# Kernel tuning notes

Hardware: AMD Instinct MI355X
Metric: run time of the kernel (lower is better)

Reference implementation:

```python
import jax, jax.numpy as jnp
import numpy as np

B, T, C = 4, 128, 512
NH, HS = 8, 64          # n_head, head_dim = C // NH
ORDER = 3               # attention_order
SCALE = 1.0 / np.sqrt(HS)


def setup_inputs() -> dict:
    key = jax.random.key(0)
    ks = jax.random.split(key, 7)
    s = 0.02
    return {
        "x": jax.random.normal(ks[0], (B, T, C), jnp.float32),
        "Wp0": jax.random.normal(ks[1], (C, C), jnp.float32) * s,
        "Wp1": jax.random.normal(ks[2], (C, C), jnp.float32) * s,
        "Wp2": jax.random.normal(ks[3], (C, C), jnp.float32) * s,
        "Wv0": jax.random.normal(ks[4], (HS, HS), jnp.float32) * s,
        "Wv1": jax.random.normal(ks[5], (HS, HS), jnp.float32) * s,
        "Wc": jax.random.normal(ks[6], (C, C), jnp.float32) * s,
    }


def _heads(x, W):
    # Linear then split heads: (B,T,C) -> (B,NH,T,HS)
    return (x @ W).reshape(B, T, NH, HS).transpose(0, 2, 1, 3)


def _causal_mask(t, order):
    # indices grid [T]^order, True where i0 >= i1 >= ... >= i_{order-1}
    idx = jnp.arange(t)
    g = jnp.stack(jnp.meshgrid(*([idx] * order), indexing='ij'), axis=-1)
    return jnp.all(jnp.diff(g, axis=-1) <= 0, axis=-1)


def reference(x, Wp0, Wp1, Wp2, Wv0, Wv1, Wc):
    p0 = _heads(x, Wp0)  # (B,NH,T,HS)
    p1 = _heads(x, Wp1)
    p2 = _heads(x, Wp2)

    # pairwise scores, then higher-order broadcast exactly as the torch einsum
    # ('bh...i,bhkd->bh...ik' sums the key over d and broadcasts — faithful).
    att = jnp.einsum('bhid,bhjd->bhij', p0, p1) * SCALE        # (B,NH,T,T)
    att = jnp.einsum('bh...i,bhkd->bh...ik', att, p2)          # (B,NH,T,T,T)

    mask = _causal_mask(T, ORDER)[None, None]                  # (1,1,T,T,T)
    att = jnp.where(mask, att, -jnp.inf)
    att = jax.nn.softmax(att.reshape(B, NH, T, T * T), axis=-1)

    # value tensors with broadcasted elementwise product over the order dims
    V0 = (p1 @ Wv0)[:, :, :, None, :]   # (B,NH,T,1,HS)
    V1 = (p2 @ Wv1)[:, :, None, :, :]   # (B,NH,1,T,HS)
    V = (V0 * V1).reshape(B, NH, T * T, HS)

    y = jnp.einsum('bhij,bhjd->bhid', att, V)                  # (B,NH,T,HS)
    y = y.transpose(0, 2, 1, 3).reshape(B, T, C)
    return y @ Wc
```

## Files before the change

### kernel.cpp

```cpp
#include <hip/hip_runtime.h>
#include <hip/hip_bf16.h>
#include <math.h>

#define B 4
#define T 128
#define C 512
#define NH 8
#define HS 64
#define BH (B*NH)

typedef __attribute__((ext_vector_type(8))) short bf16x8;
typedef __attribute__((ext_vector_type(4))) float f32x4;

__device__ __forceinline__ unsigned short bfc(float x) {
    return __builtin_bit_cast(unsigned short, __float2bfloat16(x));
}
__device__ __forceinline__ unsigned int pk_bf16(float a, float b) {
    return (unsigned int)bfc(a) | ((unsigned int)bfc(b) << 16);
}
__device__ __forceinline__ float lo_f(unsigned int g) {
    return __builtin_bit_cast(float, g << 16);
}
__device__ __forceinline__ float hi_f(unsigned int g) {
    return __builtin_bit_cast(float, g & 0xffff0000u);
}

__global__ __launch_bounds__(256) void proj_kernel(
    const float* __restrict__ X,
    const float* __restrict__ Wp0, const float* __restrict__ Wp1, const float* __restrict__ Wp2,
    unsigned short* __restrict__ p0b, unsigned short* __restrict__ p1b,
    unsigned short* __restrict__ p2b, float* __restrict__ rr)
{
    __shared__ __align__(16) unsigned short As[32][72];
    __shared__ __align__(16) unsigned short Bs[64][72];
    __shared__ float Ls[64][69];
    __shared__ float sRS[4][32];
    const int z = blockIdx.z;
    const float* W = (z == 0) ? Wp0 : (z == 1) ? Wp1 : Wp2;
    const int m0 = blockIdx.y * 32, n0 = blockIdx.x * 64;
    const int tid = threadIdx.x;
    const int w = tid >> 6, lane = tid & 63, quad = lane >> 4, l16 = lane & 15;
    f32x4 acc[2];
    #pragma unroll
    for (int mt = 0; mt < 2; ++mt) acc[mt] = (f32x4){0.f, 0.f, 0.f, 0.f};

    for (int k0 = 0; k0 < 512; k0 += 64) {
        __syncthreads();
        {
            const int row = tid >> 3, c8 = (tid & 7) * 8;
            const float4 a = *(const float4*)&X[(size_t)(m0 + row) * 512 + k0 + c8];
            const float4 b = *(const float4*)&X[(size_t)(m0 + row) * 512 + k0 + c8 + 4];
            uint4 o;
            o.x = pk_bf16(a.x, a.y);
            o.y = pk_bf16(a.z, a.w);
            o.z = pk_bf16(b.x, b.y);
            o.w = pk_bf16(b.z, b.w);
            *(uint4*)&As[row][c8] = o;
        }
        #pragma unroll
        for (int it = 0; it < 4; ++it) {
            const int q = tid + it * 256;
            const int row = q >> 4, c4 = (q & 15) * 4;
            const float4 v = *(const float4*)&W[(size_t)(k0 + row) * 512 + n0 + c4];
            Ls[row][c4 + 0] = v.x; Ls[row][c4 + 1] = v.y;
            Ls[row][c4 + 2] = v.z; Ls[row][c4 + 3] = v.w;
        }
        __syncthreads();
        #pragma unroll
        for (int it = 0; it < 2; ++it) {
            const int q = tid + it * 256;
            const int nrow = q >> 3, k8 = (q & 7) * 8;
            uint4 o;
            o.x = pk_bf16(Ls[k8 + 0][nrow], Ls[k8 + 1][nrow]);
            o.y = pk_bf16(Ls[k8 + 2][nrow], Ls[k8 + 3][nrow]);
            o.z = pk_bf16(Ls[k8 + 4][nrow], Ls[k8 + 5][nrow]);
            o.w = pk_bf16(Ls[k8 + 6][nrow], Ls[k8 + 7][nrow]);
            *(uint4*)&Bs[nrow][k8] = o;
        }
        __syncthreads();
        #pragma unroll
        for (int kt = 0; kt < 2; ++kt) {
            const bf16x8 b8 = *(const bf16x8*)&Bs[w * 16 + l16][kt * 32 + quad * 8];
            #pragma unroll
            for (int mt = 0; mt < 2; ++mt) {
                const bf16x8 a8 = *(const bf16x8*)&As[mt * 16 + l16][kt * 32 + quad * 8];
                acc[mt] = __builtin_amdgcn_mfma_f32_16x16x32_bf16(a8, b8, acc[mt], 0, 0, 0);
            }
        }
    }

    {
        const int n = n0 + w * 16 + l16;
        const int h = n >> 6, d = n & 63;
        unsigned short* pz = (z == 0) ? p0b : (z == 1) ? p1b : p2b;
        #pragma unroll
        for (int mt = 0; mt < 2; ++mt) {
            #pragma unroll
            for (int r = 0; r < 4; ++r) {
                const int m = m0 + mt * 16 + quad * 4 + r;
                const int bb = m >> 7, t = m & 127;
                pz[((size_t)(bb * NH + h) * T + t) * HS + d] = bfc(acc[mt][r]);
            }
        }
    }
    if (z == 2) {
        #pragma unroll
        for (int mt = 0; mt < 2; ++mt)
            #pragma unroll
            for (int r = 0; r < 4; ++r) {
                float v = acc[mt][r];
                v += __shfl_xor(v, 1, 64); v += __shfl_xor(v, 2, 64);
                v += __shfl_xor(v, 4, 64); v += __shfl_xor(v, 8, 64);
                if (l16 == 0) sRS[w][mt * 16 + quad * 4 + r] = v;
            }
        __syncthreads();
        if (tid < 32) {
            const float s = sRS[0][tid] + sRS[1][tid] + sRS[2][tid] + sRS[3][tid];
            const int m = m0 + tid, bb = m >> 7, tl = m & 127, h = n0 >> 6;
            rr[(bb * NH + h) * T + tl] = s;
        }
    }
}

__global__ __launch_bounds__(512, 4) void attn_kernel(
    const unsigned short* __restrict__ p0b, const unsigned short* __restrict__ p1b,
    const unsigned short* __restrict__ p2b, const float* __restrict__ rr,
    const float* __restrict__ Wv0, const float* __restrict__ Wv1,
    unsigned short* __restrict__ Yb)
{
    __shared__ __align__(16) union {
        struct {
            unsigned short sWv[64][72];
            unsigned short sVst[64][136];
        } v;
        unsigned short sE[2][128 * 128];
    } u;
    __shared__ float sS[8][128];
    __shared__ float srr[128];
    __shared__ float sZarr[8][8];
    __shared__ float sY[8][2][64];

    const int bid = blockIdx.x;
    const int bh = bid & (BH - 1);
    const int ig = bid >> 5;
    const int tid = threadIdx.x;
    const int w = tid >> 6;
    const int lane = tid & 63;
    const int quad = lane >> 4;
    const int l16 = lane & 15;
    const int wq = w & 3;
    const int h4 = (w >> 2) * 4;

    if (tid < 128) srr[tid] = rr[bh * T + tid];

    #pragma unroll
    for (int it = 0; it < 2; ++it) {
        const int k = (tid >> 4) + it * 32;
        const int d0 = (tid & 15) * 4;
        const float4 wv = *(const float4*)&Wv0[(size_t)k * 64 + d0];
        u.v.sWv[d0 + 0][k] = bfc(wv.x); u.v.sWv[d0 + 1][k] = bfc(wv.y);
        u.v.sWv[d0 + 2][k] = bfc(wv.z); u.v.sWv[d0 + 3][k] = bfc(wv.w);
    }
    __syncthreads();

    {
        f32x4 vacc[4];
        #pragma unroll
        for (int mt = 0; mt < 4; ++mt) vacc[mt] = (f32x4){0.f, 0.f, 0.f, 0.f};
        #pragma unroll
        for (int kt = 0; kt < 2; ++kt) {
            const bf16x8 b8 = *(const bf16x8*)&p1b[((size_t)bh * T + w * 16 + l16) * HS + kt * 32 + quad * 8];
            #pragma unroll
            for (int mt = 0; mt < 4; ++mt) {
                const bf16x8 a8 = *(const bf16x8*)&u.v.sWv[mt * 16 + l16][kt * 32 + quad * 8];
                vacc[mt] = __builtin_amdgcn_mfma_f32_16x16x32_bf16(a8, b8, vacc[mt], 0, 0, 0);
            }
        }
        #pragma unroll
        for (int mt = 0; mt < 4; ++mt)
            #pragma unroll
            for (int r = 0; r < 4; ++r)
                u.v.sVst[mt * 16 + quad * 4 + r][w * 16 + l16] = bfc(vacc[mt][r]);
    }
    __syncthreads();

    uint2 v0r[4];
    #pragma unroll
    for (int m = 0; m < 4; ++m)
        v0r[m] = *(const uint2*)&u.v.sVst[(wq << 4) + l16][((h4 + m) << 4) + (quad << 2)];
    #pragma unroll
    for (int it = 0; it < 2; ++it) {
        const int k = (tid >> 4) + it * 32;
        const int d0 = (tid & 15) * 4;
        const float4 wv = *(const float4*)&Wv1[(size_t)k * 64 + d0];
        u.v.sWv[d0 + 0][k] = bfc(wv.x); u.v.sWv[d0 + 1][k] = bfc(wv.y);
        u.v.sWv[d0 + 2][k] = bfc(wv.z); u.v.sWv[d0 + 3][k] = bfc(wv.w);
    }
    __syncthreads();

    {
        f32x4 vacc[4];
        #pragma unroll
        for (int mt = 0; mt < 4; ++mt) vacc[mt] = (f32x4){0.f, 0.f, 0.f, 0.f};
        #pragma unroll
        for (int kt = 0; kt < 2; ++kt) {
            const bf16x8 b8 = *(const bf16x8*)&p2b[((size_t)bh * T + w * 16 + l16) * HS + kt * 32 + quad * 8];
            #pragma unroll
            for (int mt = 0; mt < 4; ++mt) {
                const bf16x8 a8 = *(const bf16x8*)&u.v.sWv[mt * 16 + l16][kt * 32 + quad * 8];
                vacc[mt] = __builtin_amdgcn_mfma_f32_16x16x32_bf16(a8, b8, vacc[mt], 0, 0, 0);
            }
        }
        #pragma unroll
        for (int mt = 0; mt < 4; ++mt)
            #pragma unroll
            for (int r = 0; r < 4; ++r)
                u.v.sVst[mt * 16 + quad * 4 + r][w * 16 + l16] = bfc(vacc[mt][r]);
    }
    __syncthreads();

    uint4 v1r[4];
    #pragma unroll
    for (int kt = 0; kt < 4; ++kt)
        v1r[kt] = *(const uint4*)&u.v.sVst[(wq << 4) + l16][(quad << 3) + (kt << 5)];
    {
        const int qr = l16 & 7;
        const int irow = (qr & 1) ? (16 * qr + 15 - ig) : (16 * qr + ig);
        const unsigned short* ap = p0b + ((size_t)bh * T + irow) * HS + (quad << 3);
        const unsigned short* bp = p1b + (size_t)bh * T * HS + (quad << 3);
        f32x4 s0 = (f32x4){0.f, 0.f, 0.f, 0.f};
        #pragma unroll
        for (int kt = 0; kt < 2; ++kt) {
            const bf16x8 a8 = *(const bf16x8*)(ap + (kt << 5));
            const bf16x8 b0 = *(const bf16x8*)(bp + (size_t)((w << 4) + l16) * HS + (kt << 5));
            s0 = __builtin_amdgcn_mfma_f32_16x16x32_bf16(a8, b0, s0, 0, 0, 0);
        }
        if (quad < 2) {
            #pragma unroll
            for (int r = 0; r < 4; ++r)
                sS[quad * 4 + r][(w << 4) + l16] = s0[r] * 0.125f;
        }
    }
    __syncthreads();

    const float L2E = 1.4426950408889634f;

    float mhat;
    {
        float aS = 0.f;
        #pragma unroll
        for (int q = 0; q < 8; ++q) {
            aS = fmaxf(aS, fabsf(sS[q][lane]));
            aS = fmaxf(aS, fabsf(sS[q][64 + lane]));
        }
        float aR = fmaxf(fabsf(srr[lane]), fabsf(srr[64 + lane]));
        #pragma unroll
        for (int off = 32; off; off >>= 1) {
            aS = fmaxf(aS, __shfl_xor(aS, off, 64));
            aR = fmaxf(aR, __shfl_xor(aR, off, 64));
        }
        mhat = aS * aR;
    }
    const float bexp = -mhat * L2E;
    const int cc = tid & 15;
    const int rowin = tid >> 4;
    const int k0l = cc << 3;
    float rk[8];
    *(float4*)&rk[0] = *(const float4*)&srr[k0l];
    *(float4*)&rk[4] = *(const float4*)&srr[k0l + 4];

    for (int qq = 7; qq >= 0; --qq) {
        const int i = (qq & 1) ? (16 * qq + 15 - ig) : (16 * qq + ig);
        const float* sSq = sS[qq];
        const int mtmax = i >> 4;
        const int buf = qq & 1;
        float zacc = 0.f;

        const int npass = (mtmax + 2) >> 1;
        for (int p = 0; p < npass; ++p) {
            const int jj = (p << 5) + rowin;
            uint4 o = {0u, 0u, 0u, 0u};
            if (jj <= i && k0l <= jj) {
                const float aL = sSq[jj] * L2E;
                const int dlim = jj - k0l;
                float e[8];
                #pragma unroll
                for (int q = 0; q < 8; ++q) {
                    const float ex = __builtin_amdgcn_exp2f(fmaf(aL, rk[q], bexp));
                    e[q] = (q <= dlim) ? ex : 0.f;
                    zacc += e[q];
                }
                o.x = pk_bf16(e[0], e[1]);
                o.y = pk_bf16(e[2], e[3]);
                o.z = pk_bf16(e[4], e[5]);
                o.w = pk_bf16(e[6], e[7]);
            }
            *(uint4*)&u.sE[buf][(jj << 7) + ((cc ^ (jj & 7)) << 3)] = o;
        }
        #pragma unroll
        for (int off = 32; off; off >>= 1) zacc += __shfl_xor(zacc, off, 64);
        if (lane == 0) sZarr[qq][w] = zacc;
        __syncthreads();

        f32x4 acc[4];
        #pragma unroll
        for (int m = 0; m < 4; ++m) acc[m] = (f32x4){0.f, 0.f, 0.f, 0.f};
        #pragma unroll
        for (int mtl = 0; mtl < 4; ++mtl) {
            const int mt = h4 + mtl;
            if (mt <= mtmax) {
                #pragma unroll
                for (int kt = 0; kt < 4; ++kt) {
                    if (kt <= (mt >> 1)) {
                        const int ch = ((kt << 2) + quad) ^ (l16 & 7);
                        const bf16x8 a8 = *(const bf16x8*)&u.sE[buf][(((mt << 4) + l16) << 7) + (ch << 3)];
                        acc[mtl] = __builtin_amdgcn_mfma_f32_16x16x32_bf16(
                            a8, __builtin_bit_cast(bf16x8, v1r[kt]), acc[mtl], 0, 0, 0);
                    }
                }
            }
        }

        float part = 0.f;
        #pragma unroll
        for (int mtl = 0; mtl < 4; ++mtl) {
            const int mt = h4 + mtl;
            if (mt < mtmax) {
                const uint2 uu = v0r[mtl];
                part = fmaf(lo_f(uu.x), acc[mtl][0], part);
                part = fmaf(hi_f(uu.x), acc[mtl][1], part);
                part = fmaf(lo_f(uu.y), acc[mtl][2], part);
                part = fmaf(hi_f(uu.y), acc[mtl][3], part);
            } else if (mt == mtmax) {
                const uint2 uu = v0r[mtl];
                const int jb = (mt << 4) + (quad << 2);
                if (jb + 0 <= i) part = fmaf(lo_f(uu.x), acc[mtl][0], part);
                if (jb + 1 <= i) part = fmaf(hi_f(uu.x), acc[mtl][1], part);
                if (jb + 2 <= i) part = fmaf(lo_f(uu.y), acc[mtl][2], part);
                if (jb + 3 <= i) part = fmaf(hi_f(uu.y), acc[mtl][3], part);
            }
        }
        part += __shfl_xor(part, 16, 64);
        part += __shfl_xor(part, 32, 64);
        if (lane < 16) sY[qq][w >> 2][(wq << 4) + l16] = part;
    }

    __syncthreads();
    {
        const int qq = w;
        const int d = lane;
        const int i = (qq & 1) ? (16 * qq + 15 - ig) : (16 * qq + ig);
        float Z = 0.f;
        #pragma unroll
        for (int ww = 0; ww < 8; ++ww) Z += sZarr[qq][ww];
        const float y = sY[qq][0][d] + sY[qq][1][d];
        const int bb = bh >> 3, hh = bh & 7;
        Yb[((size_t)(bb * T + i) * C) + hh * HS + d] = bfc(y / Z);
    }
}

__global__ __launch_bounds__(256) void outmm_kernel(
    const unsigned short* __restrict__ Ab, const float* __restrict__ Wc,
    float* __restrict__ OUT)
{
    __shared__ __align__(16) unsigned short As[32][72];
    __shared__ __align__(16) unsigned short Bs[64][72];
    __shared__ float Ls[64][69];
    const int m0 = blockIdx.y * 32, n0 = blockIdx.x * 64;
    const int tid = threadIdx.x;
    const int w = tid >> 6, lane = tid & 63, quad = lane >> 4, l16 = lane & 15;
    f32x4 acc[2];
    #pragma unroll
    for (int mt = 0; mt < 2; ++mt) acc[mt] = (f32x4){0.f, 0.f, 0.f, 0.f};
    for (int k0 = 0; k0 < 512; k0 += 64) {
        __syncthreads();
        {
            const int row = tid >> 3, c8 = (tid & 7) * 8;
            *(uint4*)&As[row][c8] = *(const uint4*)&Ab[(size_t)(m0 + row) * 512 + k0 + c8];
        }
        #pragma unroll
        for (int it = 0; it < 4; ++it) {
            const int q = tid + it * 256;
            const int row = q >> 4, c4 = (q & 15) * 4;
            const float4 v = *(const float4*)&Wc[(size_t)(k0 + row) * 512 + n0 + c4];
            Ls[row][c4 + 0] = v.x; Ls[row][c4 + 1] = v.y;
            Ls[row][c4 + 2] = v.z; Ls[row][c4 + 3] = v.w;
        }
        __syncthreads();
        #pragma unroll
        for (int it = 0; it < 2; ++it) {
            const int q = tid + it * 256;
            const int nrow = q >> 3, k8 = (q & 7) * 8;
            uint4 o;
            o.x = pk_bf16(Ls[k8 + 0][nrow], Ls[k8 + 1][nrow]);
            o.y = pk_bf16(Ls[k8 + 2][nrow], Ls[k8 + 3][nrow]);
            o.z = pk_bf16(Ls[k8 + 4][nrow], Ls[k8 + 5][nrow]);
            o.w = pk_bf16(Ls[k8 + 6][nrow], Ls[k8 + 7][nrow]);
            *(uint4*)&Bs[nrow][k8] = o;
        }
        __syncthreads();
        #pragma unroll
        for (int kt = 0; kt < 2; ++kt) {
            const bf16x8 b8 = *(const bf16x8*)&Bs[w * 16 + l16][kt * 32 + quad * 8];
            #pragma unroll
            for (int mt = 0; mt < 2; ++mt) {
                const bf16x8 a8 = *(const bf16x8*)&As[mt * 16 + l16][kt * 32 + quad * 8];
                acc[mt] = __builtin_amdgcn_mfma_f32_16x16x32_bf16(a8, b8, acc[mt], 0, 0, 0);
            }
        }
    }
    const int n = n0 + w * 16 + l16;
    #pragma unroll
    for (int mt = 0; mt < 2; ++mt)
        #pragma unroll
        for (int r = 0; r < 4; ++r) {
            const int mrow = m0 + mt * 16 + quad * 4 + r;
            OUT[(size_t)mrow * 512 + n] = acc[mt][r];
        }
}

extern "C" void kernel_launch(void* const* d_in, const int* in_sizes, int n_in,
                              void* d_out, int out_size, void* d_ws, size_t ws_size,
                              hipStream_t stream)
{
    const float* x   = (const float*)d_in[0];
    const float* Wp0 = (const float*)d_in[1];
    const float* Wp1 = (const float*)d_in[2];
    const float* Wp2 = (const float*)d_in[3];
    const float* Wv0 = (const float*)d_in[4];
    const float* Wv1 = (const float*)d_in[5];
    const float* Wc  = (const float*)d_in[6];
    float* out = (float*)d_out;

    char* w8 = (char*)d_ws;
    const size_t HB = 512 * 1024;
    unsigned short* p0b = (unsigned short*)(w8 + 0 * HB);
    unsigned short* p1b = (unsigned short*)(w8 + 1 * HB);
    unsigned short* p2b = (unsigned short*)(w8 + 2 * HB);
    unsigned short* Yb  = (unsigned short*)(w8 + 3 * HB);
    float*          rr  = (float*)        (w8 + 4 * HB);

    proj_kernel <<<dim3(8, 16, 3), 256, 0, stream>>>(x, Wp0, Wp1, Wp2, p0b, p1b, p2b, rr);
    attn_kernel <<<dim3(512), 512, 0, stream>>>(p0b, p1b, p2b, rr, Wv0, Wv1, Yb);
    outmm_kernel<<<dim3(8, 16), 256, 0, stream>>>(Yb, Wc, out);
}
```

Before: 111.1 us.

## Keep softmax exponent tiles in registers as MFMA operands, dropping LDS staging

The attention kernel now builds the exp tile for each row directly in registers and feeds it as the A operand of the MFMA. This replaces the double-buffered shared-memory sE tile and the per-query-row __syncthreads. Each warp owns a 16-row j-block and skips query rows below its block. Partial outputs are reduced later through a larger sY buffer. This removes LDS writes and reads and per-iteration barriers, at the cost of unbalanced work across warps (warp 0 runs all 8 rows, warp 7 only one) and more V operand reads from LDS.

```diff
diff --git a/kernel.cpp b/kernel.cpp
--- a/kernel.cpp
+++ b/kernel.cpp
@@ -128,17 +128,15 @@
     const float* __restrict__ Wv0, const float* __restrict__ Wv1,
     unsigned short* __restrict__ Yb)
 {
+    __shared__ __align__(16) unsigned short sV0T[64][136];
+    __shared__ __align__(16) unsigned short sV1T[64][136];
     __shared__ __align__(16) union {
-        struct {
-            unsigned short sWv[64][72];
-            unsigned short sVst[64][136];
-        } v;
-        unsigned short sE[2][128 * 128];
-    } u;
+        unsigned short sWv[64][72];
+        float sY[8][8][64];
+    } u2;
     __shared__ float sS[8][128];
     __shared__ float srr[128];
     __shared__ float sZarr[8][8];
-    __shared__ float sY[8][2][64];
 
     const int bid = blockIdx.x;
     const int bh = bid & (BH - 1);
@@ -148,8 +146,6 @@
     const int lane = tid & 63;
     const int quad = lane >> 4;
     const int l16 = lane & 15;
-    const int wq = w & 3;
-    const int h4 = (w >> 2) * 4;
 
     if (tid < 128) srr[tid] = rr[bh * T + tid];
 
@@ -158,8 +154,8 @@
         const int k = (tid >> 4) + it * 32;
         const int d0 = (tid & 15) * 4;
         const float4 wv = *(const float4*)&Wv0[(size_t)k * 64 + d0];
-        u.v.sWv[d0 + 0][k] = bfc(wv.x); u.v.sWv[d0 + 1][k] = bfc(wv.y);
-        u.v.sWv[d0 + 2][k] = bfc(wv.z); u.v.sWv[d0 + 3][k] = bfc(wv.w);
+        u2.sWv[d0 + 0][k] = bfc(wv.x); u2.sWv[d0 + 1][k] = bfc(wv.y);
+        u2.sWv[d0 + 2][k] = bfc(wv.z); u2.sWv[d0 + 3][k] = bfc(wv.w);
     }
     __syncthreads();
 
@@ -172,7 +168,7 @@
             const bf16x8 b8 = *(const bf16x8*)&p1b[((size_t)bh * T + w * 16 + l16) * HS + kt * 32 + quad * 8];
             #pragma unroll
             for (int mt = 0; mt < 4; ++mt) {
-                const bf16x8 a8 = *(const bf16x8*)&u.v.sWv[mt * 16 + l16][kt * 32 + quad * 8];
+                const bf16x8 a8 = *(const bf16x8*)&u2.sWv[mt * 16 + l16][kt * 32 + quad * 8];
                 vacc[mt] = __builtin_amdgcn_mfma_f32_16x16x32_bf16(a8, b8, vacc[mt], 0, 0, 0);
             }
         }
@@ -180,21 +176,17 @@
         for (int mt = 0; mt < 4; ++mt)
             #pragma unroll
             for (int r = 0; r < 4; ++r)
-                u.v.sVst[mt * 16 + quad * 4 + r][w * 16 + l16] = bfc(vacc[mt][r]);
-    }
-    __syncthreads();
-
-    uint2 v0r[4];
-    #pragma unroll
-    for (int m = 0; m < 4; ++m)
-        v0r[m] = *(const uint2*)&u.v.sVst[(wq << 4) + l16][((h4 + m) << 4) + (quad << 2)];
+                sV0T[mt * 16 + quad * 4 + r][w * 16 + l16] = bfc(vacc[mt][r]);
+    }
+    __syncthreads();
+
     #pragma unroll
     for (int it = 0; it < 2; ++it) {
         const int k = (tid >> 4) + it * 32;
         const int d0 = (tid & 15) * 4;
         const float4 wv = *(const float4*)&Wv1[(size_t)k * 64 + d0];
-        u.v.sWv[d0 + 0][k] = bfc(wv.x); u.v.sWv[d0 + 1][k] = bfc(wv.y);
-        u.v.sWv[d0 + 2][k] = bfc(wv.z); u.v.sWv[d0 + 3][k] = bfc(wv.w);
+        u2.sWv[d0 + 0][k] = bfc(wv.x); u2.sWv[d0 + 1][k] = bfc(wv.y);
+        u2.sWv[d0 + 2][k] = bfc(wv.z); u2.sWv[d0 + 3][k] = bfc(wv.w);
     }
     __syncthreads();
 
@@ -207,7 +199,7 @@
             const bf16x8 b8 = *(const bf16x8*)&p2b[((size_t)bh * T + w * 16 + l16) * HS + kt * 32 + quad * 8];
             #pragma unroll
             for (int mt = 0; mt < 4; ++mt) {
-                const bf16x8 a8 = *(const bf16x8*)&u.v.sWv[mt * 16 + l16][kt * 32 + quad * 8];
+                const bf16x8 a8 = *(const bf16x8*)&u2.sWv[mt * 16 + l16][kt * 32 + quad * 8];
                 vacc[mt] = __builtin_amdgcn_mfma_f32_16x16x32_bf16(a8, b8, vacc[mt], 0, 0, 0);
             }
         }
@@ -215,14 +207,10 @@
         for (int mt = 0; mt < 4; ++mt)
             #pragma unroll
             for (int r = 0; r < 4; ++r)
-                u.v.sVst[mt * 16 + quad * 4 + r][w * 16 + l16] = bfc(vacc[mt][r]);
-    }
-    __syncthreads();
-
-    uint4 v1r[4];
-    #pragma unroll
-    for (int kt = 0; kt < 4; ++kt)
-        v1r[kt] = *(const uint4*)&u.v.sVst[(wq << 4) + l16][(quad << 3) + (kt << 5)];
+                sV1T[mt * 16 + quad * 4 + r][w * 16 + l16] = bfc(vacc[mt][r]);
+    }
+    __syncthreads();
+
     {
         const int qr = l16 & 7;
         const int irow = (qr & 1) ? (16 * qr + 15 - ig) : (16 * qr + ig);
@@ -241,6 +229,9 @@
                 sS[quad * 4 + r][(w << 4) + l16] = s0[r] * 0.125f;
         }
     }
+    #pragma unroll
+    for (int it = 0; it < 8; ++it) ((float*)u2.sY)[tid + it * 512] = 0.f;
+    if (tid < 64) ((float*)sZarr)[tid] = 0.f;
     __syncthreads();
 
     const float L2E = 1.4426950408889634f;
@@ -262,100 +253,85 @@
         mhat = aS * aR;
     }
     const float bexp = -mhat * L2E;
-    const int cc = tid & 15;
-    const int rowin = tid >> 4;
-    const int k0l = cc << 3;
-    float rk[8];
-    *(float4*)&rk[0] = *(const float4*)&srr[k0l];
-    *(float4*)&rk[4] = *(const float4*)&srr[k0l + 4];
-
-    for (int qq = 7; qq >= 0; --qq) {
+    const int jrow = (w << 4) + l16;
+    const int ktmax = w >> 1;
+
+    for (int qq = 7; qq >= w; --qq) {
         const int i = (qq & 1) ? (16 * qq + 15 - ig) : (16 * qq + ig);
-        const float* sSq = sS[qq];
-        const int mtmax = i >> 4;
-        const int buf = qq & 1;
+        const float aL = sS[qq][jrow] * L2E;
+        const bool rowok = (jrow <= i);
+        f32x4 acc[4];
+        #pragma unroll
+        for (int dt = 0; dt < 4; ++dt) acc[dt] = (f32x4){0.f, 0.f, 0.f, 0.f};
         float zacc = 0.f;
 
-        const int npass = (mtmax + 2) >> 1;
-        for (int p = 0; p < npass; ++p) {
-            const int jj = (p << 5) + rowin;
-            uint4 o = {0u, 0u, 0u, 0u};
-            if (jj <= i && k0l <= jj) {
-                const float aL = sSq[jj] * L2E;
-                const int dlim = jj - k0l;
-                float e[8];
-                #pragma unroll
-                for (int q = 0; q < 8; ++q) {
-                    const float ex = __builtin_amdgcn_exp2f(fmaf(aL, rk[q], bexp));
-                    e[q] = (q <= dlim) ? ex : 0.f;
-                    zacc += e[q];
-                }
-                o.x = pk_bf16(e[0], e[1]);
-                o.y = pk_bf16(e[2], e[3]);
-                o.z = pk_bf16(e[4], e[5]);
-                o.w = pk_bf16(e[6], e[7]);
-            }
-            *(uint4*)&u.sE[buf][(jj << 7) + ((cc ^ (jj & 7)) << 3)] = o;
-        }
+        for (int kt = 0; kt <= ktmax; ++kt) {
+            const int kbase = (kt << 5) + (quad << 3);
+            float rk[8];
+            *(float4*)&rk[0] = *(const float4*)&srr[kbase];
+            *(float4*)&rk[4] = *(const float4*)&srr[kbase + 4];
+            const int dlim = rowok ? (jrow - kbase) : -1;
+            float e[8];
+            #pragma unroll
+            for (int q = 0; q < 8; ++q) {
+                const float ex = __builtin_amdgcn_exp2f(fmaf(aL, rk[q], bexp));
+                e[q] = (q <= dlim) ? ex : 0.f;
+                zacc += e[q];
+            }
+            uint4 o;
+            o.x = pk_bf16(e[0], e[1]);
+            o.y = pk_bf16(e[2], e[3]);
+            o.z = pk_bf16(e[4], e[5]);
+            o.w = pk_bf16(e[6], e[7]);
+            const bf16x8 a8 = __builtin_bit_cast(bf16x8, o);
+            #pragma unroll
+            for (int dt = 0; dt < 4; ++dt) {
+                const bf16x8 b8 = *(const bf16x8*)&sV1T[(dt << 4) + l16][(quad << 3) + (kt << 5)];
+                acc[dt] = __builtin_amdgcn_mfma_f32_16x16x32_bf16(a8, b8, acc[dt], 0, 0, 0);
+            }
+        }
+
+        float part[4];
+        #pragma unroll
+        for (int dt = 0; dt < 4; ++dt) {
+            const uint2 uu = *(const uint2*)&sV0T[(dt << 4) + l16][(w << 4) + (quad << 2)];
+            float p = 0.f;
+            if (w < qq) {
+                p = fmaf(lo_f(uu.x), acc[dt][0], p);
+                p = fmaf(hi_f(uu.x), acc[dt][1], p);
+                p = fmaf(lo_f(uu.y), acc[dt][2], p);
+                p = fmaf(hi_f(uu.y), acc[dt][3], p);
+            } else {
+                const int jb = (w << 4) + (quad << 2);
+                if (jb + 0 <= i) p = fmaf(lo_f(uu.x), acc[dt][0], p);
+                if (jb + 1 <= i) p = fmaf(hi_f(uu.x), acc[dt][1], p);
+                if (jb + 2 <= i) p = fmaf(lo_f(uu.y), acc[dt][2], p);
+                if (jb + 3 <= i) p = fmaf(hi_f(uu.y), acc[dt][3], p);
+            }
+            p += __shfl_xor(p, 16, 64);
+            p += __shfl_xor(p, 32, 64);
+            part[dt] = p;
+        }
+        const float sel = (quad == 0) ? part[0] : (quad == 1) ? part[1] : (quad == 2) ? part[2] : part[3];
+        u2.sY[qq][w][lane] = sel;
+
         #pragma unroll
         for (int off = 32; off; off >>= 1) zacc += __shfl_xor(zacc, off, 64);
         if (lane == 0) sZarr[qq][w] = zacc;
-        __syncthreads();
-
-        f32x4 acc[4];
-        #pragma unroll
-        for (int m = 0; m < 4; ++m) acc[m] = (f32x4){0.f, 0.f, 0.f, 0.f};
-        #pragma unroll
-        for (int mtl = 0; mtl < 4; ++mtl) {
-            const int mt = h4 + mtl;
-            if (mt <= mtmax) {
-                #pragma unroll
-                for (int kt = 0; kt < 4; ++kt) {
-                    if (kt <= (mt >> 1)) {
-                        const int ch = ((kt << 2) + quad) ^ (l16 & 7);
-                        const bf16x8 a8 = *(const bf16x8*)&u.sE[buf][(((mt << 4) + l16) << 7) + (ch << 3)];
-                        acc[mtl] = __builtin_amdgcn_mfma_f32_16x16x32_bf16(
-                            a8, __builtin_bit_cast(bf16x8, v1r[kt]), acc[mtl], 0, 0, 0);
-                    }
-                }
-            }
-        }
-
-        float part = 0.f;
-        #pragma unroll
-        for (int mtl = 0; mtl < 4; ++mtl) {
-            const int mt = h4 + mtl;
-            if (mt < mtmax) {
-                const uint2 uu = v0r[mtl];
-                part = fmaf(lo_f(uu.x), acc[mtl][0], part);
-                part = fmaf(hi_f(uu.x), acc[mtl][1], part);
-                part = fmaf(lo_f(uu.y), acc[mtl][2], part);
-                part = fmaf(hi_f(uu.y), acc[mtl][3], part);
-            } else if (mt == mtmax) {
-                const uint2 uu = v0r[mtl];
-                const int jb = (mt << 4) + (quad << 2);
-                if (jb + 0 <= i) part = fmaf(lo_f(uu.x), acc[mtl][0], part);
-                if (jb + 1 <= i) part = fmaf(hi_f(uu.x), acc[mtl][1], part);
-                if (jb + 2 <= i) part = fmaf(lo_f(uu.y), acc[mtl][2], part);
-                if (jb + 3 <= i) part = fmaf(hi_f(uu.y), acc[mtl][3], part);
-            }
-        }
-        part += __shfl_xor(part, 16, 64);
-        part += __shfl_xor(part, 32, 64);
-        if (lane < 16) sY[qq][w >> 2][(wq << 4) + l16] = part;
-    }
-
-    __syncthreads();
+    }
+    __syncthreads();
+
     {
         const int qq = w;
-        const int d = lane;
         const int i = (qq & 1) ? (16 * qq + 15 - ig) : (16 * qq + ig);
         float Z = 0.f;
         #pragma unroll
         for (int ww = 0; ww < 8; ++ww) Z += sZarr[qq][ww];
-        const float y = sY[qq][0][d] + sY[qq][1][d];
+        float y = 0.f;
+        #pragma unroll
+        for (int ww = 0; ww < 8; ++ww) y += u2.sY[qq][ww][lane];
         const int bb = bh >> 3, hh = bh & 7;
-        Yb[((size_t)(bb * T + i) * C) + hh * HS + d] = bfc(y / Z);
+        Yb[((size_t)(bb * T + i) * C) + hh * HS + lane] = bfc(y / Z);
     }
 }
 
```

Result: faster. 104.0 us (-6.5%).
